# Optimization experiments

Hardware: AMD Instinct MI355X
Metric: run time of the kernel (lower is better)

## Reference

```python
import jax, jax.numpy as jnp
import numpy as np

EPS = 1e-12  # matches torch F.normalize eps default

def _l2_normalize(x, axis=-1):
    n = jnp.linalg.norm(x, axis=axis, keepdims=True)
    return x / jnp.maximum(n, EPS)

def setup_inputs() -> dict:
    key = jax.random.key(0)
    k1, k2, k3 = jax.random.split(key, 3)
    B, N, D = 1024, 500000, 128
    return {
        "query_embeddings": jax.random.normal(k1, (B, D), dtype=jnp.float32),
        "memory_keys": jax.random.normal(k2, (N, D), dtype=jnp.float32),
        "memory_values": jax.random.normal(k3, (N, D), dtype=jnp.float32),
        "top_k": 8,
    }

def reference(query_embeddings, memory_keys, memory_values, top_k):
    # L2-normalize queries and memory keys (torch F.normalize, p=2)
    q = _l2_normalize(query_embeddings, axis=1)        # [B, D]
    k = _l2_normalize(memory_keys, axis=1)             # [N, D]
    # Cosine similarities: [B, N]
    sims = jnp.einsum('bd,nd->bn', q, k)
    # Top-k (largest, sorted) per query
    _, topk_idx = jax.lax.top_k(sims, top_k)           # [B, k]
    # Gather values: [B, k, D]
    retrieved = memory_values[topk_idx]
    return retrieved
```

## Files before the change

kernel.cpp:

```cpp
#include <hip/hip_runtime.h>


#define DIM 128
#define TOPK 8
#define THR0 0.30f
#define CHUNKS 128
#define QPB 256
#define NCAND 24

typedef _Float16 half8 __attribute__((ext_vector_type(8)));
typedef _Float16 half2v __attribute__((ext_vector_type(2)));
typedef float f32x4 __attribute__((ext_vector_type(4)));

__global__ __launch_bounds__(256) void norm_rows_kernel(const float* __restrict__ in,
                                                        _Float16* __restrict__ outh,
                                                        int rows) {
  int row = blockIdx.x * 4 + (threadIdx.x >> 6);
  int lane = threadIdx.x & 63;
  if (row >= rows) return;
  float2 v = *(const float2*)(in + (size_t)row * DIM + lane * 2);
  float ss = v.x * v.x + v.y * v.y;
#pragma unroll
  for (int off = 32; off; off >>= 1) ss += __shfl_xor(ss, off);
  float inv = 1.0f / fmaxf(sqrtf(ss), 1e-12f);
  half2v o;
  o.x = (_Float16)(v.x * inv);
  o.y = (_Float16)(v.y * inv);
  *(half2v*)(outh + (size_t)row * DIM + lane * 2) = o;
}

__global__ __launch_bounds__(1024) void score_select_kernel(
    const _Float16* __restrict__ qh, const _Float16* __restrict__ kh,
    float* __restrict__ cscore, int* __restrict__ cidx, int N, int iters) {
  __shared__ _Float16 ktile[2][64 * 136];
  __shared__ float lscore[QPB * 8];
  __shared__ int lidx[QPB * 8];
  __shared__ float thrL[QPB];

  const int tid = threadIdx.x;
  const int lane = tid & 63;
  const int w = tid >> 6;
  const int col = lane & 15;
  const int quad = lane >> 4;
  const int qg = blockIdx.x;
  const int chunk = blockIdx.y;
  const long chunk_base = (long)chunk * iters * 64;

  for (int e = tid; e < QPB * 8; e += 1024) {
    lscore[e] = -1e30f;
    lidx[e] = 0;
  }
  if (tid < QPB) thrL[tid] = THR0;

  half8 bf[4];
  {
    const _Float16* qrow = qh + ((size_t)qg * QPB + w * 16 + col) * DIM + quad * 8;
#pragma unroll
    for (int t = 0; t < 4; t++) bf[t] = *(const half8*)(qrow + t * 32);
  }

  const int srow = tid >> 4;
  const int scol = tid & 15;
  const int ld_off = srow * 136 + scol * 8;

  float4 staged;
  {
    long key = chunk_base + srow;
    if (key < (long)N)
      staged = *(const float4*)(kh + key * (size_t)DIM + scol * 8);
    else
      staged.x = staged.y = staged.z = staged.w = 0.f;
  }

  float thr_cur = THR0;
  for (int it = 0; it < iters; ++it) {
    *(float4*)(ktile[it & 1] + ld_off) = staged;
    __syncthreads();
    if (it + 1 < iters) {
      long key = chunk_base + (long)(it + 1) * 64 + srow;
      if (key < (long)N)
        staged = *(const float4*)(kh + key * (size_t)DIM + scol * 8);
      else
        staged.x = staged.y = staged.z = staged.w = 0.f;
    }
    const _Float16* kt = ktile[it & 1];
    const long keyb_it = chunk_base + (long)it * 64;
#pragma unroll
    for (int sub = 0; sub < 4; ++sub) {
      const _Float16* arow = kt + (sub * 16 + col) * 136 + quad * 8;
      f32x4 acc = {0.f, 0.f, 0.f, 0.f};
#pragma unroll
      for (int t = 0; t < 4; t++) {
        half8 af = *(const half8*)(arow + t * 32);
        acc = __builtin_amdgcn_mfma_f32_16x16x32_f16(af, bf[t], acc, 0, 0, 0);
      }
      float mx = fmaxf(fmaxf(acc[0], acc[1]), fmaxf(acc[2], acc[3]));
      if (__any(mx > thr_cur)) {
        const long keyb = keyb_it + sub * 16;
#pragma unroll
        for (int r = 0; r < 4; ++r) {
          float av = acc[r];
          unsigned long long m = __ballot(av > thr_cur);
          while (m) {
            int src = __ffsll(m) - 1;
            m &= m - 1;
            float sc = __shfl(av, src);
            int qq = w * 16 + (src & 15);
            long kk = keyb + (src >> 4) * 4 + r;
            if (lane == 0 && kk < (long)N) {
              float* Ls = lscore + qq * 8;
              int* Li = lidx + qq * 8;
              float mn = Ls[0];
              int ms = 0;
#pragma unroll
              for (int s2 = 1; s2 < 8; s2++) {
                float vv = Ls[s2];
                if (vv < mn) { mn = vv; ms = s2; }
              }
              if (sc > mn) {
                Ls[ms] = sc;
                Li[ms] = (int)kk;
                float nm = Ls[0];
#pragma unroll
                for (int s2 = 1; s2 < 8; s2++) nm = fminf(nm, Ls[s2]);
                thrL[qq] = fmaxf(THR0, nm);
              }
            }
          }
        }
        thr_cur = thrL[w * 16 + col];
      }
    }
  }
  __syncthreads();
  for (int e = tid; e < QPB * 8; e += 1024) {
    int ql = e >> 3, slot = e & 7;
    size_t o = ((size_t)qg * QPB + ql) * (CHUNKS * 8) + (size_t)chunk * 8 + slot;
    cscore[o] = lscore[e];
    cidx[o] = lidx[e];
  }
}

__global__ __launch_bounds__(64) void merge_rescore_kernel(
    const float* __restrict__ Q, const float* __restrict__ Kf, const float* __restrict__ V,
    const float* __restrict__ cscore, const int* __restrict__ cidx,
    float* __restrict__ out, int N) {
  const int q = blockIdx.x;
  const int lane = threadIdx.x;
  const int E = CHUNKS * 8;
  float s[16];
  int ii[16];
#pragma unroll
  for (int i = 0; i < 16; i++) {
    size_t o = (size_t)q * E + i * 64 + lane;
    s[i] = cscore[o];
    ii[i] = cidx[o];
  }
  __shared__ int topI[NCAND];
  __shared__ double simsL[NCAND];
  unsigned consumed = 0;
  for (int t = 0; t < NCAND; t++) {
    float bv = -3e38f;
    int bid = 0x7fffffff;
    int bpos = -1;
#pragma unroll
    for (int i = 0; i < 16; i++) {
      float v = ((consumed >> i) & 1) ? -3e38f : s[i];
      if (v > bv || (v == bv && ii[i] < bid)) { bv = v; bid = ii[i]; bpos = i; }
    }
    float myv = bv;
    int myi = bid;
#pragma unroll
    for (int off = 32; off; off >>= 1) {
      float ov = __shfl_xor(bv, off);
      int oi = __shfl_xor(bid, off);
      if (ov > bv || (ov == bv && oi < bid)) { bv = ov; bid = oi; }
    }
    if (bv <= -1e29f) {
      if (lane == 0)
        for (int z = t; z < NCAND; z++) topI[z] = -1;
      break;
    }
    if (bpos >= 0 && myv == bv && myi == bid) consumed |= 1u << bpos;
    if (lane == 0) topI[t] = bid;
  }
  __syncthreads();

  float q0 = Q[(size_t)q * DIM + lane];
  float q1 = Q[(size_t)q * DIM + 64 + lane];
  double dq = (double)q0 * q0 + (double)q1 * q1;
#pragma unroll
  for (int off = 32; off; off >>= 1) dq += __shfl_xor(dq, off);
  double qn = fmax(sqrt(dq), 1e-12);
  for (int c = 0; c < NCAND; ++c) {
    int id = topI[c];
    int idc = id < 0 ? 0 : id;
    float kx = Kf[(size_t)idc * DIM + lane];
    float ky = Kf[(size_t)idc * DIM + 64 + lane];
    double dot = (double)q0 * kx + (double)q1 * ky;
    double ks = (double)kx * kx + (double)ky * ky;
#pragma unroll
    for (int off = 32; off; off >>= 1) {
      dot += __shfl_xor(dot, off);
      ks += __shfl_xor(ks, off);
    }
    double sim = dot / (qn * fmax(sqrt(ks), 1e-12));
    if (lane == 0) simsL[c] = (id >= 0) ? sim : -1e300;
  }
  __syncthreads();

  unsigned used = 0;
  for (int j = 0; j < TOPK; j++) {
    double bv = -1e301;
    int bc = -1;
    int bid = 0x7fffffff;
    for (int c = 0; c < NCAND; c++) {
      if ((used >> c) & 1) continue;
      int id = topI[c];
      if (id < 0) continue;
      double v = simsL[c];
      if (v > bv || (v == bv && id < bid)) { bv = v; bid = id; bc = c; }
    }
    int row = 0;
    if (bc >= 0) {
      used |= 1u << bc;
      row = topI[bc];
    }
    out[((size_t)q * TOPK + j) * DIM + lane] = V[(size_t)row * DIM + lane];
    out[((size_t)q * TOPK + j) * DIM + 64 + lane] = V[(size_t)row * DIM + 64 + lane];
  }
}

extern "C" void kernel_launch(void* const* d_in, const int* in_sizes, int n_in,
                              void* d_out, int out_size, void* d_ws, size_t ws_size,
                              hipStream_t stream) {
  const float* Q = (const float*)d_in[0];
  const float* Kf = (const float*)d_in[1];
  const float* V = (const float*)d_in[2];
  float* out = (float*)d_out;
  const int B = in_sizes[0] / DIM;
  const int N = in_sizes[1] / DIM;

  char* ws = (char*)d_ws;
  size_t cand_elems = (size_t)B * CHUNKS * 8;
  float* cscore = (float*)ws;
  int* cidx = (int*)(ws + cand_elems * 4);
  _Float16* qh = (_Float16*)(ws + cand_elems * 8);
  _Float16* kh = (_Float16*)(ws + cand_elems * 8 + (size_t)B * DIM * 2);

  int iters = (N + CHUNKS * 64 - 1) / (CHUNKS * 64);

  norm_rows_kernel<<<dim3((B + 3) / 4), 256, 0, stream>>>(Q, qh, B);
  norm_rows_kernel<<<dim3((N + 3) / 4), 256, 0, stream>>>(Kf, kh, N);
  score_select_kernel<<<dim3(B / QPB, CHUNKS), 1024, 0, stream>>>(qh, kh, cscore, cidx, N, iters);
  merge_rescore_kernel<<<dim3(B), 64, 0, stream>>>(Q, Kf, V, cscore, cidx, out, N);
}
```

Before: 699.1 us.

## Restructure score kernel: per-wave 4 query tiles, XOR-swizzled LDS, global candidate lists

```diff
diff --git a/kernel.cpp b/kernel.cpp
--- a/kernel.cpp
+++ b/kernel.cpp
@@ -4,64 +4,71 @@
 #define DIM 128
 #define TOPK 8
 #define THR0 0.30f
-#define CHUNKS 128
+#define NCH 64
 #define QPB 256
+#define SLOTS 32
 #define NCAND 24
 
 typedef _Float16 half8 __attribute__((ext_vector_type(8)));
-typedef _Float16 half2v __attribute__((ext_vector_type(2)));
+typedef _Float16 half4v __attribute__((ext_vector_type(4)));
 typedef float f32x4 __attribute__((ext_vector_type(4)));
 
 __global__ __launch_bounds__(256) void norm_rows_kernel(const float* __restrict__ in,
                                                         _Float16* __restrict__ outh,
                                                         int rows) {
-  int row = blockIdx.x * 4 + (threadIdx.x >> 6);
-  int lane = threadIdx.x & 63;
+  int row = blockIdx.x * 8 + (threadIdx.x >> 5);
+  int l = threadIdx.x & 31;
   if (row >= rows) return;
-  float2 v = *(const float2*)(in + (size_t)row * DIM + lane * 2);
-  float ss = v.x * v.x + v.y * v.y;
-#pragma unroll
-  for (int off = 32; off; off >>= 1) ss += __shfl_xor(ss, off);
+  float4 v = *(const float4*)(in + (size_t)row * DIM + l * 4);
+  float ss = v.x * v.x + v.y * v.y + v.z * v.z + v.w * v.w;
+#pragma unroll
+  for (int off = 16; off; off >>= 1) ss += __shfl_xor(ss, off);
   float inv = 1.0f / fmaxf(sqrtf(ss), 1e-12f);
-  half2v o;
+  half4v o;
   o.x = (_Float16)(v.x * inv);
   o.y = (_Float16)(v.y * inv);
-  *(half2v*)(outh + (size_t)row * DIM + lane * 2) = o;
-}
-
-__global__ __launch_bounds__(1024) void score_select_kernel(
+  o.z = (_Float16)(v.z * inv);
+  o.w = (_Float16)(v.w * inv);
+  *(half4v*)(outh + (size_t)row * DIM + l * 4) = o;
+}
+
+__global__ __launch_bounds__(1024, 4) void score_select_kernel(
     const _Float16* __restrict__ qh, const _Float16* __restrict__ kh,
-    float* __restrict__ cscore, int* __restrict__ cidx, int N, int iters) {
-  __shared__ _Float16 ktile[2][64 * 136];
-  __shared__ float lscore[QPB * 8];
-  __shared__ int lidx[QPB * 8];
-  __shared__ float thrL[QPB];
+    float* cscore, int* cidx, int N, int iters) {
+  __shared__ _Float16 ktile[2][64 * 128];
+  __shared__ float thrL[1024];
 
   const int tid = threadIdx.x;
   const int lane = tid & 63;
   const int w = tid >> 6;
   const int col = lane & 15;
   const int quad = lane >> 4;
+  const int ks = w & 3;
+  const int qgrp = w >> 2;
   const int qg = blockIdx.x;
   const int chunk = blockIdx.y;
   const long chunk_base = (long)chunk * iters * 64;
 
-  for (int e = tid; e < QPB * 8; e += 1024) {
-    lscore[e] = -1e30f;
-    lidx[e] = 0;
-  }
-  if (tid < QPB) thrL[tid] = THR0;
-
-  half8 bf[4];
+  for (int e = tid; e < QPB * SLOTS; e += 1024) {
+    size_t o = ((size_t)(qg * QPB + (e >> 5))) * (NCH * SLOTS) + (size_t)chunk * SLOTS + (e & 31);
+    cscore[o] = -1e30f;
+    cidx[o] = 0;
+  }
+  thrL[tid & 1023] = THR0;
+
+  half8 bf[4][4];
   {
-    const _Float16* qrow = qh + ((size_t)qg * QPB + w * 16 + col) * DIM + quad * 8;
-#pragma unroll
-    for (int t = 0; t < 4; t++) bf[t] = *(const half8*)(qrow + t * 32);
+    const _Float16* qbase = qh + ((size_t)qg * QPB + qgrp * 64 + col) * DIM + quad * 8;
+#pragma unroll
+    for (int qt = 0; qt < 4; qt++)
+#pragma unroll
+      for (int t = 0; t < 4; t++)
+        bf[qt][t] = *(const half8*)(qbase + qt * 16 * DIM + t * 32);
   }
 
   const int srow = tid >> 4;
   const int scol = tid & 15;
-  const int ld_off = srow * 136 + scol * 8;
+  const int st_off = srow * 128 + ((scol ^ (srow & 15)) * 8);
 
   float4 staged;
   {
@@ -72,9 +79,10 @@
       staged.x = staged.y = staged.z = staged.w = 0.f;
   }
 
-  float thr_cur = THR0;
+  float thr_c[4] = {THR0, THR0, THR0, THR0};
+
   for (int it = 0; it < iters; ++it) {
-    *(float4*)(ktile[it & 1] + ld_off) = staged;
+    *(float4*)(&ktile[it & 1][st_off]) = staged;
     __syncthreads();
     if (it + 1 < iters) {
       long key = chunk_base + (long)(it + 1) * 64 + srow;
@@ -84,60 +92,61 @@
         staged.x = staged.y = staged.z = staged.w = 0.f;
     }
     const _Float16* kt = ktile[it & 1];
-    const long keyb_it = chunk_base + (long)it * 64;
-#pragma unroll
-    for (int sub = 0; sub < 4; ++sub) {
-      const _Float16* arow = kt + (sub * 16 + col) * 136 + quad * 8;
-      f32x4 acc = {0.f, 0.f, 0.f, 0.f};
-#pragma unroll
-      for (int t = 0; t < 4; t++) {
-        half8 af = *(const half8*)(arow + t * 32);
-        acc = __builtin_amdgcn_mfma_f32_16x16x32_f16(af, bf[t], acc, 0, 0, 0);
-      }
-      float mx = fmaxf(fmaxf(acc[0], acc[1]), fmaxf(acc[2], acc[3]));
-      if (__any(mx > thr_cur)) {
-        const long keyb = keyb_it + sub * 16;
+    const int arow = (ks * 16 + col) * 128;
+
+    f32x4 acc[4];
+#pragma unroll
+    for (int qt = 0; qt < 4; qt++) acc[qt] = (f32x4){0.f, 0.f, 0.f, 0.f};
+#pragma unroll
+    for (int t = 0; t < 4; t++) {
+      half8 af = *(const half8*)(kt + arow + (((quad + 4 * t) ^ col) * 8));
+#pragma unroll
+      for (int qt = 0; qt < 4; qt++)
+        acc[qt] = __builtin_amdgcn_mfma_f32_16x16x32_f16(af, bf[qt][t], acc[qt], 0, 0, 0);
+    }
+
+    const long keyb = chunk_base + (long)it * 64 + ks * 16;
+#pragma unroll
+    for (int qt = 0; qt < 4; qt++) {
+      float mx = fmaxf(fmaxf(acc[qt][0], acc[qt][1]), fmaxf(acc[qt][2], acc[qt][3]));
+      if (__any(mx > thr_c[qt])) {
 #pragma unroll
         for (int r = 0; r < 4; ++r) {
-          float av = acc[r];
-          unsigned long long m = __ballot(av > thr_cur);
+          float av = acc[qt][r];
+          unsigned long long m = __ballot(av > thr_c[qt]);
           while (m) {
             int src = __ffsll(m) - 1;
             m &= m - 1;
             float sc = __shfl(av, src);
-            int qq = w * 16 + (src & 15);
+            int qq = qgrp * 64 + qt * 16 + (src & 15);
             long kk = keyb + (src >> 4) * 4 + r;
             if (lane == 0 && kk < (long)N) {
-              float* Ls = lscore + qq * 8;
-              int* Li = lidx + qq * 8;
-              float mn = Ls[0];
+              size_t base = ((size_t)(qg * QPB + qq)) * (NCH * SLOTS) + (size_t)chunk * SLOTS + ks * 8;
+              float* Ls = cscore + base;
+              int* Li = cidx + base;
+              float lv[8];
+#pragma unroll
+              for (int s2 = 0; s2 < 8; s2++) lv[s2] = Ls[s2];
+              float mn = lv[0];
               int ms = 0;
 #pragma unroll
-              for (int s2 = 1; s2 < 8; s2++) {
-                float vv = Ls[s2];
-                if (vv < mn) { mn = vv; ms = s2; }
-              }
+              for (int s2 = 1; s2 < 8; s2++)
+                if (lv[s2] < mn) { mn = lv[s2]; ms = s2; }
               if (sc > mn) {
                 Ls[ms] = sc;
                 Li[ms] = (int)kk;
-                float nm = Ls[0];
-#pragma unroll
-                for (int s2 = 1; s2 < 8; s2++) nm = fminf(nm, Ls[s2]);
-                thrL[qq] = fmaxf(THR0, nm);
+                lv[ms] = sc;
+                float nm = lv[0];
+#pragma unroll
+                for (int s2 = 1; s2 < 8; s2++) nm = fminf(nm, lv[s2]);
+                thrL[ks * 256 + qq] = fmaxf(THR0, nm);
               }
             }
           }
         }
-        thr_cur = thrL[w * 16 + col];
+        thr_c[qt] = thrL[ks * 256 + qgrp * 64 + qt * 16 + col];
       }
     }
-  }
-  __syncthreads();
-  for (int e = tid; e < QPB * 8; e += 1024) {
-    int ql = e >> 3, slot = e & 7;
-    size_t o = ((size_t)qg * QPB + ql) * (CHUNKS * 8) + (size_t)chunk * 8 + slot;
-    cscore[o] = lscore[e];
-    cidx[o] = lidx[e];
   }
 }
 
@@ -147,11 +156,11 @@
     float* __restrict__ out, int N) {
   const int q = blockIdx.x;
   const int lane = threadIdx.x;
-  const int E = CHUNKS * 8;
-  float s[16];
-  int ii[16];
-#pragma unroll
-  for (int i = 0; i < 16; i++) {
+  const int E = NCH * SLOTS;
+  float s[32];
+  int ii[32];
+#pragma unroll
+  for (int i = 0; i < 32; i++) {
     size_t o = (size_t)q * E + i * 64 + lane;
     s[i] = cscore[o];
     ii[i] = cidx[o];
@@ -164,7 +173,7 @@
     int bid = 0x7fffffff;
     int bpos = -1;
 #pragma unroll
-    for (int i = 0; i < 16; i++) {
+    for (int i = 0; i < 32; i++) {
       float v = ((consumed >> i) & 1) ? -3e38f : s[i];
       if (v > bv || (v == bv && ii[i] < bid)) { bv = v; bid = ii[i]; bpos = i; }
     }
@@ -198,13 +207,13 @@
     float kx = Kf[(size_t)idc * DIM + lane];
     float ky = Kf[(size_t)idc * DIM + 64 + lane];
     double dot = (double)q0 * kx + (double)q1 * ky;
-    double ks = (double)kx * kx + (double)ky * ky;
+    double ksq = (double)kx * kx + (double)ky * ky;
 #pragma unroll
     for (int off = 32; off; off >>= 1) {
       dot += __shfl_xor(dot, off);
-      ks += __shfl_xor(ks, off);
-    }
-    double sim = dot / (qn * fmax(sqrt(ks), 1e-12));
+      ksq += __shfl_xor(ksq, off);
+    }
+    double sim = dot / (qn * fmax(sqrt(ksq), 1e-12));
     if (lane == 0) simsL[c] = (id >= 0) ? sim : -1e300;
   }
   __syncthreads();
@@ -242,16 +251,16 @@
   const int N = in_sizes[1] / DIM;
 
   char* ws = (char*)d_ws;
-  size_t cand_elems = (size_t)B * CHUNKS * 8;
+  size_t cand_elems = (size_t)B * NCH * SLOTS;
   float* cscore = (float*)ws;
   int* cidx = (int*)(ws + cand_elems * 4);
   _Float16* qh = (_Float16*)(ws + cand_elems * 8);
   _Float16* kh = (_Float16*)(ws + cand_elems * 8 + (size_t)B * DIM * 2);
 
-  int iters = (N + CHUNKS * 64 - 1) / (CHUNKS * 64);
-
-  norm_rows_kernel<<<dim3((B + 3) / 4), 256, 0, stream>>>(Q, qh, B);
-  norm_rows_kernel<<<dim3((N + 3) / 4), 256, 0, stream>>>(Kf, kh, N);
-  score_select_kernel<<<dim3(B / QPB, CHUNKS), 1024, 0, stream>>>(qh, kh, cscore, cidx, N, iters);
+  int iters = (N + NCH * 64 - 1) / (NCH * 64);
+
+  norm_rows_kernel<<<dim3((B + 7) / 8), 256, 0, stream>>>(Q, qh, B);
+  norm_rows_kernel<<<dim3((N + 7) / 8), 256, 0, stream>>>(Kf, kh, N);
+  score_select_kernel<<<dim3(B / QPB, NCH), 1024, 0, stream>>>(qh, kh, cscore, cidx, N, iters);
   merge_rescore_kernel<<<dim3(B), 64, 0, stream>>>(Q, Kf, V, cscore, cidx, out, N);
 }
```

New measurement: 759.3 us. 1.09x slower.
